# Performance work log

Measured on AMD Instinct MI355X. Metric: run time of the kernel, lower is better.

Reference implementation:

```python
import jax, jax.numpy as jnp
import numpy as np
from jax import lax

N, C, H, W = 4, 256, 64, 64
R = 2          # upsample ratio (scale_factor)
K = 5          # CARAFE up_kernel
COMP = 64      # CARAFEPack compressed_channels
EPS = 1e-5     # BatchNorm eps


def setup_inputs() -> dict:
    key = jax.random.key(0)
    ks = jax.random.split(key, 8)
    w = lambda k, s: jax.random.normal(k, s, jnp.float32) * 0.05
    return {
        "low_feature": jax.random.normal(ks[0], (N, C, H * R, W * R), jnp.float32),
        "high_feature": jax.random.normal(ks[1], (N, C, H, W), jnp.float32),
        "w_cc": w(ks[2], (COMP, C, 1, 1)),            # channel compressor 1x1
        "b_cc": jnp.zeros((COMP,), jnp.float32),
        "w_ce": w(ks[3], (K * K * R * R, COMP, 3, 3)), # content encoder 3x3
        "b_ce": jnp.zeros((K * K * R * R,), jnp.float32),
        "w_conv2": w(ks[4], (C, C, 1, 1)),
        "b_conv2": jnp.zeros((C,), jnp.float32),
        "w_bott": w(ks[5], (C, 2 * C, 1, 1)),          # bottleneck 1x1, no bias
        "gamma": jnp.ones((C,), jnp.float32),
        "beta": jnp.zeros((C,), jnp.float32),
    }


def _conv1x1(x, w, b=None):
    y = jnp.einsum('nchw,oc->nohw', x, w[:, :, 0, 0])
    if b is not None:
        y = y + b[None, :, None, None]
    return y


def _conv3x3(x, w, b):
    y = lax.conv_general_dilated(x, w, (1, 1), [(1, 1), (1, 1)],
                                 dimension_numbers=('NCHW', 'OIHW', 'NCHW'))
    return y + b[None, :, None, None]


def _pixel_shuffle(x, r):
    n, c, h, w = x.shape
    c2 = c // (r * r)
    x = x.reshape(n, c2, r, r, h, w).transpose(0, 1, 4, 2, 5, 3)
    return x.reshape(n, c2, h * r, w * r)


def _carafe(x, w_cc, b_cc, w_ce, b_ce):
    n, c, h, w = x.shape
    # predicted kernels: compress -> encode -> pixel_shuffle -> softmax over k^2
    mask = _conv3x3(_conv1x1(x, w_cc, b_cc), w_ce, b_ce)      # [N, K*K*R*R, H, W]
    mask = _pixel_shuffle(mask, R)                            # [N, K*K, H*R, W*R]
    mask = jax.nn.softmax(mask, axis=1)                       # group=1 -> over K*K
    # k x k neighborhoods of x (zero-padded), kernel index = ky*K + kx
    pad = K // 2
    xp = jnp.pad(x, ((0, 0), (0, 0), (pad, pad), (pad, pad)))
    patches = jnp.stack([xp[:, :, dy:dy + h, dx:dx + w]
                         for dy in range(K) for dx in range(K)], axis=2)  # [N,C,K*K,H,W]
    # each output pixel (i,j) reads source (i//R, j//R) neighborhood
    mr = mask.reshape(n, K * K, h, R, w, R)
    out = jnp.einsum('nckhw,nkhawb->nchawb', patches, mr)
    return out.reshape(n, c, h * R, w * R)


def reference(low_feature, high_feature, w_cc, b_cc, w_ce, b_ce,
              w_conv2, b_conv2, w_bott, gamma, beta):
    hf = _carafe(high_feature, w_cc, b_cc, w_ce, b_ce)        # [N,C,H*R,W*R]
    value = _conv1x1(hf, w_conv2, b_conv2)
    x = jnp.concatenate([value, hf], axis=1)                  # [N,2C,.,.]
    x = _conv1x1(x, w_bott)
    # BatchNorm (training-mode batch statistics) + ReLU
    mean = jnp.mean(x, axis=(0, 2, 3), keepdims=True)
    var = jnp.var(x, axis=(0, 2, 3), keepdims=True)
    x = (x - mean) * lax.rsqrt(var + EPS)
    x = x * gamma[None, :, None, None] + beta[None, :, None, None]
    return jax.nn.relu(x)
```

## Files before the change

### kernel.cpp

```cpp
#include <hip/hip_runtime.h>
#include <hip/hip_bf16.h>

#define N_    4
#define C_    256
#define PS_   4096
#define PO_   16384
#define COMP_ 64
#define QCH_  100

typedef unsigned short u16;
typedef __attribute__((ext_vector_type(8))) short short8;
typedef __attribute__((ext_vector_type(4))) float f32x4;

__device__ __forceinline__ u16 f2bu(float f) {
    __hip_bfloat16 h = __float2bfloat16(f);
    return __builtin_bit_cast(u16, h);
}
__device__ __forceinline__ float bits2f(unsigned u) {
    union { unsigned i; float f; } v; v.i = u; return v.f;
}

__global__ __launch_bounds__(256) void k_prep(const float* __restrict__ w_bott,
        const float* __restrict__ w_conv2, const float* __restrict__ b_conv2,
        const float* __restrict__ w_ce, const float* __restrict__ w_cc,
        u16* __restrict__ Weff_bf, float* __restrict__ beff,
        u16* __restrict__ Wb, u16* __restrict__ Wcc_bf) {
    int bid = blockIdx.x;
    if (bid < 256) {
        int o = bid, c = threadIdx.x;
        __shared__ float wb[512];
        wb[c]       = w_bott[o * 512 + c];
        wb[c + 256] = w_bott[o * 512 + 256 + c];
        __syncthreads();
        float acc = wb[256 + c];
        #pragma unroll 8
        for (int m = 0; m < 256; ++m)
            acc += wb[m] * w_conv2[m * 256 + c];
        Weff_bf[o * 256 + c] = f2bu(acc);
        if (c == 0) {
            float be = 0.f;
            for (int m = 0; m < 256; ++m) be += wb[m] * b_conv2[m];
            beff[o] = be;
        }
    } else if (bid < 544) {
        int i = (bid - 256) * 256 + threadIdx.x;
        int q = i / 576, u = i - q * 576;
        float v = (q < 100) ? w_ce[q * 576 + u] : 0.f;
        Wb[i] = f2bu(v);
    } else {
        int j = (bid - 544) * 256 + threadIdx.x;
        Wcc_bf[j] = f2bu(w_cc[j]);
    }
}

__global__ __launch_bounds__(256) void k_ygemm_fused(const u16* __restrict__ Weff_bf,
        const u16* __restrict__ Wcc_bf, const float* __restrict__ high,
        const float* __restrict__ b_cc, u16* __restrict__ Yt,
        float* __restrict__ comp) {
    int tid = threadIdx.x;
    int wid = tid >> 6, lane = tid & 63;
    int col = lane & 15, quad = lane >> 4;
    int px0 = blockIdx.x * 128;
    int y = blockIdx.y;
    int o0 = y * 128;
    int n = px0 >> 12, pxb = px0 & 4095;
    __shared__ u16 As[128 * 40];
    __shared__ u16 As2[32 * 40];
    __shared__ u16 Bs[128 * 40];
    f32x4 acc[2][8] = {};
    f32x4 cacc[8] = {};
    #pragma unroll 1
    for (int k0 = 0; k0 < 256; k0 += 32) {
        __syncthreads();
        #pragma unroll
        for (int it = 0; it < 2; ++it) {
            int s = tid + it * 256;
            int row = s >> 2, seg = s & 3;
            short8 av = *reinterpret_cast<const short8*>(Weff_bf + (o0 + row) * 256 + k0 + seg * 8);
            *reinterpret_cast<short8*>(&As[row * 40 + seg * 8]) = av;
        }
        if (tid < 128) {
            int row = tid >> 2, seg = tid & 3;
            short8 av = *reinterpret_cast<const short8*>(Wcc_bf + (y * 32 + row) * 256 + k0 + seg * 8);
            *reinterpret_cast<short8*>(&As2[row * 40 + seg * 8]) = av;
        }
        #pragma unroll
        for (int it = 0; it < 8; ++it) {
            int idx = it * 256 + tid;
            int c = (idx >> 7) * 2, px = idx & 127;
            const float* hp = high + (n * C_ + k0 + c) * PS_ + pxb + px;
            unsigned lo = f2bu(hp[0]);
            unsigned hi = f2bu(hp[PS_]);
            *reinterpret_cast<unsigned*>(&Bs[px * 40 + c]) = lo | (hi << 16);
        }
        __syncthreads();
        short8 a0 = *reinterpret_cast<const short8*>(&As[(wid * 32 + col) * 40 + quad * 8]);
        short8 a1 = *reinterpret_cast<const short8*>(&As[(wid * 32 + 16 + col) * 40 + quad * 8]);
        short8 a2;
        if (wid < 2)
            a2 = *reinterpret_cast<const short8*>(&As2[(wid * 16 + col) * 40 + quad * 8]);
        #pragma unroll
        for (int nt = 0; nt < 8; ++nt) {
            short8 b = *reinterpret_cast<const short8*>(&Bs[(nt * 16 + col) * 40 + quad * 8]);
            acc[0][nt] = __builtin_amdgcn_mfma_f32_16x16x32_bf16(a0, b, acc[0][nt], 0, 0, 0);
            acc[1][nt] = __builtin_amdgcn_mfma_f32_16x16x32_bf16(a1, b, acc[1][nt], 0, 0, 0);
            if (wid < 2)
                cacc[nt] = __builtin_amdgcn_mfma_f32_16x16x32_bf16(a2, b, cacc[nt], 0, 0, 0);
        }
    }
    #pragma unroll
    for (int mi = 0; mi < 2; ++mi) {
        int ob = o0 + wid * 32 + mi * 16 + quad * 4;
        #pragma unroll
        for (int nt = 0; nt < 8; ++nt) {
            int gpx = px0 + nt * 16 + col;
            unsigned lo = f2bu(acc[mi][nt][0]) | ((unsigned)f2bu(acc[mi][nt][1]) << 16);
            unsigned hi = f2bu(acc[mi][nt][2]) | ((unsigned)f2bu(acc[mi][nt][3]) << 16);
            uint2 pk; pk.x = lo; pk.y = hi;
            *reinterpret_cast<uint2*>(Yt + (size_t)gpx * 256 + ob) = pk;
        }
    }
    if (wid < 2) {
        #pragma unroll
        for (int r = 0; r < 4; ++r) {
            int m = y * 32 + wid * 16 + quad * 4 + r;
            float bias = b_cc[m];
            float* cp = comp + (size_t)(n * COMP_ + m) * PS_ + pxb + col;
            #pragma unroll
            for (int nt = 0; nt < 8; ++nt)
                cp[nt * 16] = cacc[nt][r] + bias;
        }
    }
}

__global__ __launch_bounds__(256) void k_im2col(const float* __restrict__ comp,
        u16* __restrict__ Icol) {
    int b = blockIdx.x;
    int n = b >> 6, tile = b & 63;
    int ty0 = (tile >> 3) << 3, tx0 = (tile & 7) << 3;
    int tid = threadIdx.x;
    __shared__ float ct[64 * 100];
    for (int idx = tid; idx < 6400; idx += 256) {
        int cc = idx / 100, r = idx - cc * 100;
        int yy = ty0 - 1 + r / 10, xx = tx0 - 1 + (r % 10);
        float v = 0.f;
        if ((unsigned)yy < 64u && (unsigned)xx < 64u)
            v = comp[(n * COMP_ + cc) * PS_ + yy * 64 + xx];
        ct[idx] = v;
    }
    __syncthreads();
    int u0 = tid * 2, u1 = u0 + 1;
    int c0 = (unsigned)u0 / 9u, t0 = u0 - c0 * 9;
    int c1 = (unsigned)u1 / 9u, t1 = u1 - c1 * 9;
    int off0 = c0 * 100 + (t0 / 3) * 10 + (t0 % 3);
    int off1 = c1 * 100 + (t1 / 3) * 10 + (t1 % 3);
    int u2 = 512 + tid * 2, u3 = u2 + 1;
    int c2 = (unsigned)u2 / 9u, t2 = u2 - c2 * 9;
    int c3 = (unsigned)u3 / 9u, t3 = u3 - c3 * 9;
    int off2 = c2 * 100 + (t2 / 3) * 10 + (t2 % 3);
    int off3 = c3 * 100 + (t3 / 3) * 10 + (t3 % 3);
    #pragma unroll 1
    for (int px = 0; px < 64; ++px) {
        int py = px >> 3, pxx = px & 7;
        int base = py * 10 + pxx;
        int gpx = n * PS_ + (ty0 + py) * 64 + tx0 + pxx;
        u16* dst = Icol + gpx * 576;
        unsigned lo = f2bu(ct[off0 + base]);
        unsigned hi = f2bu(ct[off1 + base]);
        *reinterpret_cast<unsigned*>(dst + u0) = lo | (hi << 16);
        if (tid < 32) {
            unsigned lo2 = f2bu(ct[off2 + base]);
            unsigned hi2 = f2bu(ct[off3 + base]);
            *reinterpret_cast<unsigned*>(dst + u2) = lo2 | (hi2 << 16);
        }
    }
}

__global__ __launch_bounds__(256) void k_encode_mfma(const u16* __restrict__ Wb,
        const u16* __restrict__ Icol, const float* __restrict__ b_ce,
        float* __restrict__ msm) {
    int tid = threadIdx.x;
    int wid = tid >> 6, lane = tid & 63;
    int col = lane & 15, quad = lane >> 4;
    int px0 = blockIdx.x * 64;
    int n = px0 >> 12, pxb = px0 & 4095;
    __shared__ u16 As[128 * 40];
    __shared__ u16 Bs[64 * 40];
    __shared__ float mt[100 * 64];
    f32x4 acc[2][4] = {};
    #pragma unroll 1
    for (int k0 = 0; k0 < 576; k0 += 32) {
        __syncthreads();
        #pragma unroll
        for (int it = 0; it < 2; ++it) {
            int s = tid + it * 256;
            int row = s >> 2, seg = s & 3;
            short8 av = *reinterpret_cast<const short8*>(Wb + row * 576 + k0 + seg * 8);
            *reinterpret_cast<short8*>(&As[row * 40 + seg * 8]) = av;
        }
        {
            int row = tid >> 2, seg = tid & 3;
            short8 bv = *reinterpret_cast<const short8*>(Icol + (size_t)(px0 + row) * 576 + k0 + seg * 8);
            *reinterpret_cast<short8*>(&Bs[row * 40 + seg * 8]) = bv;
        }
        __syncthreads();
        short8 a0 = *reinterpret_cast<const short8*>(&As[(wid * 32 + col) * 40 + quad * 8]);
        short8 a1 = *reinterpret_cast<const short8*>(&As[(wid * 32 + 16 + col) * 40 + quad * 8]);
        #pragma unroll
        for (int nt = 0; nt < 4; ++nt) {
            short8 b = *reinterpret_cast<const short8*>(&Bs[(nt * 16 + col) * 40 + quad * 8]);
            acc[0][nt] = __builtin_amdgcn_mfma_f32_16x16x32_bf16(a0, b, acc[0][nt], 0, 0, 0);
            acc[1][nt] = __builtin_amdgcn_mfma_f32_16x16x32_bf16(a1, b, acc[1][nt], 0, 0, 0);
        }
    }
    #pragma unroll
    for (int mi = 0; mi < 2; ++mi) {
        int qbase = (wid * 2 + mi) * 16 + quad * 4;
        #pragma unroll
        for (int r = 0; r < 4; ++r) {
            int q = qbase + r;
            if (q < 100) {
                float bias = b_ce[q];
                #pragma unroll
                for (int nt = 0; nt < 4; ++nt)
                    mt[q * 64 + nt * 16 + col] = acc[mi][nt][r] + bias;
            }
        }
    }
    __syncthreads();
    {
        int px = tid & 63, sp = tid >> 6;
        float p[25];
        float mx = -1e30f;
        #pragma unroll
        for (int k = 0; k < 25; ++k) {
            p[k] = mt[(k * 4 + sp) * 64 + px];
            mx = fmaxf(mx, p[k]);
        }
        float sum = 0.f;
        #pragma unroll
        for (int k = 0; k < 25; ++k) { p[k] = __expf(p[k] - mx); sum += p[k]; }
        float inv = 1.f / sum;
        float* mo = msm + ((size_t)n * QCH_ + sp) * PS_ + pxb + px;
        #pragma unroll
        for (int k = 0; k < 25; ++k)
            mo[(size_t)k * 4 * PS_] = p[k] * inv;
    }
}

__global__ __launch_bounds__(256) void k_carafe(const u16* __restrict__ Yt,
        const float* __restrict__ msm, const float* __restrict__ beff,
        float* __restrict__ xout, float* __restrict__ ps, float* __restrict__ pq) {
    int tile = blockIdx.x, n = blockIdx.y, half = blockIdx.z;
    int sh0 = (tile >> 3) << 3, sw0 = (tile & 7) << 3;
    int tid = threadIdx.x;
    int px = tid & 63, g = tid >> 6;
    int ly = px >> 3, lx = px & 7;
    int h = sh0 + ly, w = sw0 + lx;

    __shared__ float mt[6400];
    __shared__ u16 xt[144 * 68];

    for (int idx = tid; idx < 6400; idx += 256) {
        int q = idx >> 6, p = idx & 63;
        mt[idx] = msm[((size_t)n * QCH_ + q) * PS_ + (sh0 + (p >> 3)) * 64 + sw0 + (p & 7)];
    }
    __syncthreads();

    float vs[4][25];
    #pragma unroll
    for (int s = 0; s < 4; ++s) {
        #pragma unroll
        for (int k = 0; k < 25; ++k) vs[s][k] = mt[(k * 4 + s) * 64 + px];
    }

    const u16* Yb = Yt + (size_t)n * PS_ * 256;
    float* hp_base = xout + (size_t)(n * C_) * PO_;
    int slotbase = ((n * 64 + tile) * 2 + half) * 128;
    #pragma unroll 1
    for (int chunk = 0; chunk < 2; ++chunk) {
        int ch0 = half * 128 + chunk * 64;
        __syncthreads();
        for (int idx = tid; idx < 1152; idx += 256) {
            int sp = idx >> 3, seg = idx & 7;
            int row = sp / 12, colm = sp - row * 12;
            int yy = sh0 - 2 + row, xx = sw0 - 2 + colm;
            short8 val = {};
            if ((unsigned)yy < 64u && (unsigned)xx < 64u)
                val = *reinterpret_cast<const short8*>(Yb + (size_t)(yy * 64 + xx) * 256 + ch0 + seg * 8);
            *reinterpret_cast<short8*>(&xt[sp * 68 + seg * 8]) = val;
        }
        __syncthreads();
        #pragma unroll 1
        for (int cq = 0; cq < 4; ++cq) {
            int c = g * 16 + cq * 4;
            int ch = ch0 + c;
            f32x4 bv = *reinterpret_cast<const f32x4*>(beff + ch);
            float a_[4][4];
            #pragma unroll
            for (int s = 0; s < 4; ++s) {
                a_[s][0] = bv[0]; a_[s][1] = bv[1]; a_[s][2] = bv[2]; a_[s][3] = bv[3];
            }
            const u16* bp = xt + (ly * 12 + lx) * 68 + c;
            #pragma unroll
            for (int ky = 0; ky < 5; ++ky) {
                #pragma unroll
                for (int kx = 0; kx < 5; ++kx) {
                    uint2 rv = *reinterpret_cast<const uint2*>(bp + (ky * 12 + kx) * 68);
                    float f0 = bits2f(rv.x << 16);
                    float f1 = bits2f(rv.x & 0xffff0000u);
                    float f2 = bits2f(rv.y << 16);
                    float f3 = bits2f(rv.y & 0xffff0000u);
                    int k = ky * 5 + kx;
                    #pragma unroll
                    for (int s = 0; s < 4; ++s) {
                        float m = vs[s][k];
                        a_[s][0] += m * f0; a_[s][1] += m * f1;
                        a_[s][2] += m * f2; a_[s][3] += m * f3;
                    }
                }
            }
            #pragma unroll
            for (int i = 0; i < 4; ++i) {
                float* op = hp_base + (size_t)(ch + i) * PO_ + (2 * h) * 128 + 2 * w;
                float2 r0; r0.x = a_[0][i]; r0.y = a_[1][i];
                float2 r1; r1.x = a_[2][i]; r1.y = a_[3][i];
                *reinterpret_cast<float2*>(op) = r0;
                *reinterpret_cast<float2*>(op + 128) = r1;
            }
            f32x4 sv, qv;
            #pragma unroll
            for (int i = 0; i < 4; ++i) {
                float s  = a_[0][i] + a_[1][i] + a_[2][i] + a_[3][i];
                float q2 = a_[0][i] * a_[0][i] + a_[1][i] * a_[1][i]
                         + a_[2][i] * a_[2][i] + a_[3][i] * a_[3][i];
                #pragma unroll
                for (int off = 1; off < 64; off <<= 1) {
                    s  += __shfl_xor(s, off);
                    q2 += __shfl_xor(q2, off);
                }
                sv[i] = s; qv[i] = q2;
            }
            if ((tid & 63) == 0) {
                *reinterpret_cast<f32x4*>(ps + slotbase + chunk * 64 + c) = sv;
                *reinterpret_cast<f32x4*>(pq + slotbase + chunk * 64 + c) = qv;
            }
        }
    }
}

__global__ __launch_bounds__(256) void k_bn(const float* __restrict__ ps,
        const float* __restrict__ pq, const float* __restrict__ gamma,
        const float* __restrict__ beta, float* __restrict__ xb) {
    int o = blockIdx.x >> 2, n = blockIdx.x & 3;
    int half = o >> 7, coff = o & 127;
    int tid = threadIdx.x;
    float s = ps[(tid * 2 + half) * 128 + coff];
    float q = pq[(tid * 2 + half) * 128 + coff];
    __shared__ float rs[256], rq[256];
    rs[tid] = s; rq[tid] = q;
    __syncthreads();
    for (int off = 128; off > 0; off >>= 1) {
        if (tid < off) { rs[tid] += rs[tid + off]; rq[tid] += rq[tid + off]; }
        __syncthreads();
    }
    __shared__ float sc_s, sh_s;
    if (tid == 0) {
        float mean = rs[0] * (1.f / 65536.f);
        float var  = rq[0] * (1.f / 65536.f) - mean * mean;
        float sc = rsqrtf(var + 1e-5f) * gamma[o];
        sc_s = sc;
        sh_s = beta[o] - mean * sc;
    }
    __syncthreads();
    float sc = sc_s, sh = sh_s;
    float* p = xb + (size_t)(n * C_ + o) * PO_;
    #pragma unroll 4
    for (int i = tid * 4; i < PO_; i += 1024) {
        float4 v = *reinterpret_cast<const float4*>(p + i);
        v.x = fmaxf(v.x * sc + sh, 0.f);
        v.y = fmaxf(v.y * sc + sh, 0.f);
        v.z = fmaxf(v.z * sc + sh, 0.f);
        v.w = fmaxf(v.w * sc + sh, 0.f);
        *reinterpret_cast<float4*>(p + i) = v;
    }
}

extern "C" void kernel_launch(void* const* d_in, const int* in_sizes, int n_in,
                              void* d_out, int out_size, void* d_ws, size_t ws_size,
                              hipStream_t stream) {
    const float* high    = (const float*)d_in[1];
    const float* w_cc    = (const float*)d_in[2];
    const float* b_cc    = (const float*)d_in[3];
    const float* w_ce    = (const float*)d_in[4];
    const float* b_ce    = (const float*)d_in[5];
    const float* w_conv2 = (const float*)d_in[6];
    const float* b_conv2 = (const float*)d_in[7];
    const float* w_bott  = (const float*)d_in[8];
    const float* gamma   = (const float*)d_in[9];
    const float* beta    = (const float*)d_in[10];

    char* ws = (char*)d_ws;
    float* beff    = (float*)(ws + 0);
    u16*   Weff_bf = (u16*)  (ws + 3072);
    u16*   Wcc_bf  = (u16*)  (ws + 134144);
    u16*   Wb      = (u16*)  (ws + 166912);
    float* comp    = (float*)(ws + 314368);
    float* msm     = (float*)(ws + 4508672);
    u16*   Yt      = (u16*)  (ws + 11062272);
    float* ps      = (float*)(ws + 19450880);
    float* pq      = (float*)(ws + 19713024);
    u16*   Icol    = (u16*)  d_out;
    float* xout    = (float*)d_out;

    k_prep        <<<608, 256, 0, stream>>>(w_bott, w_conv2, b_conv2, w_ce, w_cc,
                                            Weff_bf, beff, Wb, Wcc_bf);
    k_ygemm_fused <<<dim3(128, 2), 256, 0, stream>>>(Weff_bf, Wcc_bf, high, b_cc, Yt, comp);
    k_im2col      <<<256, 256, 0, stream>>>(comp, Icol);
    k_encode_mfma <<<256, 256, 0, stream>>>(Wb, Icol, b_ce, msm);
    k_carafe      <<<dim3(64, 4, 2), 256, 0, stream>>>(Yt, msm, beff, xout, ps, pq);
    k_bn          <<<1024, 256, 0, stream>>>(ps, pq, gamma, beta, xout);
}
```

Measured before the change: 258.6 us.

## Fuse im2col into encoder GEMM and store softmax masks tile-major

Removes the separate im2col kernel. The encoder kernel now stages the zero-padded compressed tile in shared memory and builds the bf16 B operand on the fly for each K-step, so the large Icol buffer no longer makes a round trip through global memory. The softmax mask output switches to a per-tile contiguous layout, so the carafe kernel loads its mask tile as one linear copy instead of a strided gather. In exchange, each K-step now does index division and scalar LDS gathers to build B fragments, and the shared buffer is reused for both the input tile and the mask.

Result: faster. 247.8 us (-4.2%).

```diff
diff --git a/kernel.cpp b/kernel.cpp
--- a/kernel.cpp
+++ b/kernel.cpp
@@ -133,60 +133,30 @@
     }
 }
 
-__global__ __launch_bounds__(256) void k_im2col(const float* __restrict__ comp,
-        u16* __restrict__ Icol) {
+__global__ __launch_bounds__(256) void k_encode_mfma(const u16* __restrict__ Wb,
+        const float* __restrict__ comp, const float* __restrict__ b_ce,
+        float* __restrict__ msm) {
+    int tid = threadIdx.x;
+    int wid = tid >> 6, lane = tid & 63;
+    int col = lane & 15, quad = lane >> 4;
     int b = blockIdx.x;
     int n = b >> 6, tile = b & 63;
     int ty0 = (tile >> 3) << 3, tx0 = (tile & 7) << 3;
-    int tid = threadIdx.x;
-    __shared__ float ct[64 * 100];
+    __shared__ u16 As[128 * 40];
+    __shared__ u16 Bs[64 * 40];
+    __shared__ float buf[6400];
+
     for (int idx = tid; idx < 6400; idx += 256) {
         int cc = idx / 100, r = idx - cc * 100;
         int yy = ty0 - 1 + r / 10, xx = tx0 - 1 + (r % 10);
         float v = 0.f;
         if ((unsigned)yy < 64u && (unsigned)xx < 64u)
             v = comp[(n * COMP_ + cc) * PS_ + yy * 64 + xx];
-        ct[idx] = v;
-    }
-    __syncthreads();
-    int u0 = tid * 2, u1 = u0 + 1;
-    int c0 = (unsigned)u0 / 9u, t0 = u0 - c0 * 9;
-    int c1 = (unsigned)u1 / 9u, t1 = u1 - c1 * 9;
-    int off0 = c0 * 100 + (t0 / 3) * 10 + (t0 % 3);
-    int off1 = c1 * 100 + (t1 / 3) * 10 + (t1 % 3);
-    int u2 = 512 + tid * 2, u3 = u2 + 1;
-    int c2 = (unsigned)u2 / 9u, t2 = u2 - c2 * 9;
-    int c3 = (unsigned)u3 / 9u, t3 = u3 - c3 * 9;
-    int off2 = c2 * 100 + (t2 / 3) * 10 + (t2 % 3);
-    int off3 = c3 * 100 + (t3 / 3) * 10 + (t3 % 3);
-    #pragma unroll 1
-    for (int px = 0; px < 64; ++px) {
-        int py = px >> 3, pxx = px & 7;
-        int base = py * 10 + pxx;
-        int gpx = n * PS_ + (ty0 + py) * 64 + tx0 + pxx;
-        u16* dst = Icol + gpx * 576;
-        unsigned lo = f2bu(ct[off0 + base]);
-        unsigned hi = f2bu(ct[off1 + base]);
-        *reinterpret_cast<unsigned*>(dst + u0) = lo | (hi << 16);
-        if (tid < 32) {
-            unsigned lo2 = f2bu(ct[off2 + base]);
-            unsigned hi2 = f2bu(ct[off3 + base]);
-            *reinterpret_cast<unsigned*>(dst + u2) = lo2 | (hi2 << 16);
-        }
-    }
-}
-
-__global__ __launch_bounds__(256) void k_encode_mfma(const u16* __restrict__ Wb,
-        const u16* __restrict__ Icol, const float* __restrict__ b_ce,
-        float* __restrict__ msm) {
-    int tid = threadIdx.x;
-    int wid = tid >> 6, lane = tid & 63;
-    int col = lane & 15, quad = lane >> 4;
-    int px0 = blockIdx.x * 64;
-    int n = px0 >> 12, pxb = px0 & 4095;
-    __shared__ u16 As[128 * 40];
-    __shared__ u16 Bs[64 * 40];
-    __shared__ float mt[100 * 64];
+        buf[idx] = v;
+    }
+
+    int row = tid >> 2, seg = tid & 3;
+    int base = (row >> 3) * 10 + (row & 7);
     f32x4 acc[2][4] = {};
     #pragma unroll 1
     for (int k0 = 0; k0 < 576; k0 += 32) {
@@ -194,13 +164,20 @@
         #pragma unroll
         for (int it = 0; it < 2; ++it) {
             int s = tid + it * 256;
-            int row = s >> 2, seg = s & 3;
-            short8 av = *reinterpret_cast<const short8*>(Wb + row * 576 + k0 + seg * 8);
-            *reinterpret_cast<short8*>(&As[row * 40 + seg * 8]) = av;
+            int arow = s >> 2, aseg = s & 3;
+            short8 av = *reinterpret_cast<const short8*>(Wb + arow * 576 + k0 + aseg * 8);
+            *reinterpret_cast<short8*>(&As[arow * 40 + aseg * 8]) = av;
         }
         {
-            int row = tid >> 2, seg = tid & 3;
-            short8 bv = *reinterpret_cast<const short8*>(Icol + (size_t)(px0 + row) * 576 + k0 + seg * 8);
+            short8 bv;
+            #pragma unroll
+            for (int j = 0; j < 8; ++j) {
+                int u = k0 + seg * 8 + j;
+                int cc = (int)((unsigned)u / 9u);
+                int t = u - cc * 9;
+                int t3 = (int)((unsigned)t / 3u);
+                bv[j] = (short)f2bu(buf[cc * 100 + t3 * 10 + (t - t3 * 3) + base]);
+            }
             *reinterpret_cast<short8*>(&Bs[row * 40 + seg * 8]) = bv;
         }
         __syncthreads();
@@ -208,9 +185,9 @@
         short8 a1 = *reinterpret_cast<const short8*>(&As[(wid * 32 + 16 + col) * 40 + quad * 8]);
         #pragma unroll
         for (int nt = 0; nt < 4; ++nt) {
-            short8 b = *reinterpret_cast<const short8*>(&Bs[(nt * 16 + col) * 40 + quad * 8]);
-            acc[0][nt] = __builtin_amdgcn_mfma_f32_16x16x32_bf16(a0, b, acc[0][nt], 0, 0, 0);
-            acc[1][nt] = __builtin_amdgcn_mfma_f32_16x16x32_bf16(a1, b, acc[1][nt], 0, 0, 0);
+            short8 bb = *reinterpret_cast<const short8*>(&Bs[(nt * 16 + col) * 40 + quad * 8]);
+            acc[0][nt] = __builtin_amdgcn_mfma_f32_16x16x32_bf16(a0, bb, acc[0][nt], 0, 0, 0);
+            acc[1][nt] = __builtin_amdgcn_mfma_f32_16x16x32_bf16(a1, bb, acc[1][nt], 0, 0, 0);
         }
     }
     #pragma unroll
@@ -223,7 +200,7 @@
                 float bias = b_ce[q];
                 #pragma unroll
                 for (int nt = 0; nt < 4; ++nt)
-                    mt[q * 64 + nt * 16 + col] = acc[mi][nt][r] + bias;
+                    buf[q * 64 + nt * 16 + col] = acc[mi][nt][r] + bias;
             }
         }
     }
@@ -234,17 +211,17 @@
         float mx = -1e30f;
         #pragma unroll
         for (int k = 0; k < 25; ++k) {
-            p[k] = mt[(k * 4 + sp) * 64 + px];
+            p[k] = buf[(k * 4 + sp) * 64 + px];
             mx = fmaxf(mx, p[k]);
         }
         float sum = 0.f;
         #pragma unroll
         for (int k = 0; k < 25; ++k) { p[k] = __expf(p[k] - mx); sum += p[k]; }
         float inv = 1.f / sum;
-        float* mo = msm + ((size_t)n * QCH_ + sp) * PS_ + pxb + px;
+        float* mo = msm + (size_t)b * 6400;
         #pragma unroll
         for (int k = 0; k < 25; ++k)
-            mo[(size_t)k * 4 * PS_] = p[k] * inv;
+            mo[(k * 4 + sp) * 64 + px] = p[k] * inv;
     }
 }
 
@@ -261,10 +238,9 @@
     __shared__ float mt[6400];
     __shared__ u16 xt[144 * 68];
 
-    for (int idx = tid; idx < 6400; idx += 256) {
-        int q = idx >> 6, p = idx & 63;
-        mt[idx] = msm[((size_t)n * QCH_ + q) * PS_ + (sh0 + (p >> 3)) * 64 + sw0 + (p & 7)];
-    }
+    const float* msrc = msm + (size_t)(n * 64 + tile) * 6400;
+    for (int idx = tid; idx < 6400; idx += 256)
+        mt[idx] = msrc[idx];
     __syncthreads();
 
     float vs[4][25];
@@ -410,14 +386,12 @@
     u16*   Yt      = (u16*)  (ws + 11062272);
     float* ps      = (float*)(ws + 19450880);
     float* pq      = (float*)(ws + 19713024);
-    u16*   Icol    = (u16*)  d_out;
     float* xout    = (float*)d_out;
 
     k_prep        <<<608, 256, 0, stream>>>(w_bott, w_conv2, b_conv2, w_ce, w_cc,
                                             Weff_bf, beff, Wb, Wcc_bf);
     k_ygemm_fused <<<dim3(128, 2), 256, 0, stream>>>(Weff_bf, Wcc_bf, high, b_cc, Yt, comp);
-    k_im2col      <<<256, 256, 0, stream>>>(comp, Icol);
-    k_encode_mfma <<<256, 256, 0, stream>>>(Wb, Icol, b_ce, msm);
+    k_encode_mfma <<<256, 256, 0, stream>>>(Wb, comp, b_ce, msm);
     k_carafe      <<<dim3(64, 4, 2), 256, 0, stream>>>(Yt, msm, beff, xout, ps, pq);
     k_bn          <<<1024, 256, 0, stream>>>(ps, pq, gamma, beta, xout);
 }
```
